# Optimization experiments

Measured on AMD Instinct MI355X. Metric: run time of the kernel, lower is better.

Reference implementation:

```python
import jax, jax.numpy as jnp
import numpy as np


def setup_inputs() -> dict:
    key = jax.random.key(0)
    k1, k2, k3, k4, k5 = jax.random.split(key, 5)
    B, N, E, C, O = 4, 10000, 32, 128, 128
    x = jax.random.normal(k1, (B, N, C), dtype=jnp.float32)
    idx = jax.random.randint(k2, (B, N, E), 0, N)
    drop = jax.random.uniform(k3, (B, N, E)) < 0.1
    edge_index = jnp.where(drop, -1, idx).astype(jnp.int64)
    W = jax.random.normal(k4, (2 * C, O), dtype=jnp.float32) * (1.0 / np.sqrt(2 * C))
    b = jax.random.normal(k5, (O,), dtype=jnp.float32) * 0.01
    return {"x": x, "edge_index": edge_index, "W": W, "b": b}


def reference(x, edge_index, W, b):
    B, N, C = x.shape
    E = edge_index.shape[-1]
    # pad a zero node row; -1 indices point at it (torch negative-index semantics)
    padded = jnp.concatenate([x, jnp.zeros((B, 1, C), dtype=x.dtype)], axis=1)  # [B, N+1, C]
    idx = jnp.where(edge_index < 0, N, edge_index)
    neigh = jax.vmap(lambda p, i: p[i])(padded, idx)  # [B, N, E, C]
    x_e = jnp.broadcast_to(x[:, :, None, :], (B, N, E, C))
    feat = jnp.concatenate([x_e, neigh - x_e], axis=-1)  # [B, N, E, 2C]
    h = jax.nn.elu(jnp.einsum('bnec,co->bneo', feat, W) + b)  # [B, N, E, O]
    h = jnp.where((edge_index != -1)[..., None], h, -jnp.inf)
    return jnp.max(h, axis=2)  # [B, N, O]
```

## Files before the change

### kernel.cpp

```cpp
#include <hip/hip_runtime.h>
#include <math.h>

#define BATCH 4
#define NNODE 10000
#define EDIM  32
#define CDIM  128
#define ODIM  128
#define MTOT  (BATCH * NNODE)

typedef __attribute__((ext_vector_type(8))) short bf16x8;
typedef __attribute__((ext_vector_type(4))) float f32x4;

#define SENT_BF16 0xFBFFu

__device__ __forceinline__ unsigned short f2bf(float f) {
    unsigned u = __float_as_uint(f);
    u += 0x7fffu + ((u >> 16) & 1u);
    return (unsigned short)(u >> 16);
}
__device__ __forceinline__ float bf2f(unsigned short h) {
    return __uint_as_float(((unsigned)h) << 16);
}
__device__ __forceinline__ void pkmax(unsigned& acc, unsigned v) {
    asm("v_pk_max_f16 %0, %0, %1" : "+v"(acc) : "v"(v));
}

__global__ __launch_bounds__(256) void prep_w(
    const float* __restrict__ W, unsigned short* __restrict__ Bcat,
    unsigned short* __restrict__ Tsent)
{
    int gid = blockIdx.x * 256 + threadIdx.x;
    int n = gid >> 7;
    int k = gid & 127;
    float v;
    if (n < 128) v = W[(size_t)k * ODIM + n] - W[(size_t)(k + 128) * ODIM + n];
    else         v = W[(size_t)(k + 128) * ODIM + (n - 128)];
    Bcat[(size_t)n * CDIM + k] = f2bf(v);
    if (gid < ODIM) Tsent[gid] = (unsigned short)SENT_BF16;
}

__global__ __launch_bounds__(256) void gemm_mfma(
    const float* __restrict__ x,
    const unsigned short* __restrict__ Bcat,
    const float* __restrict__ bias,
    unsigned short* __restrict__ U,
    unsigned short* __restrict__ T)
{
    __shared__ unsigned short As[32 * 128];

    const int tid  = threadIdx.x;
    const int m0   = blockIdx.x * 32;
    const int wv   = tid >> 6;
    const int lane = tid & 63;
    const int l16  = lane & 15;
    const int quad = lane >> 4;
    const int nq   = wv * 64;

    #pragma unroll
    for (int i = 0; i < 4; i++) {
        int lin = i * 256 + tid;
        int row = lin >> 5;
        int f4  = lin & 31;
        float4 v = *(const float4*)&x[(size_t)(m0 + row) * CDIM + f4 * 4];
        ushort4 h;
        h.x = f2bf(v.x); h.y = f2bf(v.y); h.z = f2bf(v.z); h.w = f2bf(v.w);
        int kblk = f4 >> 1, half = f4 & 1;
        *(ushort4*)((char*)As + row * 256 + (((kblk ^ (row & 15)) << 4) + half * 8)) = h;
    }
    __syncthreads();

    f32x4 acc[2][4];
    #pragma unroll
    for (int i = 0; i < 2; i++)
        #pragma unroll
        for (int j = 0; j < 4; j++) acc[i][j] = (f32x4){0.f, 0.f, 0.f, 0.f};

    #pragma unroll
    for (int ks = 0; ks < 4; ks++) {
        const int kb = ks * 32 + quad * 8;

        bf16x8 wfr[4];
        #pragma unroll
        for (int ct = 0; ct < 4; ct++)
            wfr[ct] = *(const bf16x8*)(Bcat + (size_t)(nq + ct * 16 + l16) * CDIM + kb);

        bf16x8 xfr[2];
        #pragma unroll
        for (int rt = 0; rt < 2; rt++) {
            int row  = rt * 16 + l16;
            int kblk = ks * 4 + quad;
            xfr[rt] = *(const bf16x8*)((char*)As + row * 256 + ((kblk ^ l16) << 4));
        }

        #pragma unroll
        for (int rt = 0; rt < 2; rt++)
            #pragma unroll
            for (int ct = 0; ct < 4; ct++)
                acc[rt][ct] = __builtin_amdgcn_mfma_f32_16x16x32_bf16(
                    wfr[ct], xfr[rt], acc[rt][ct], 0, 0, 0);
    }

    if (wv < 2) {
        #pragma unroll
        for (int ct = 0; ct < 4; ct++) {
            int c0 = nq + ct * 16 + quad * 4;
            float4 b4 = *(const float4*)&bias[c0];
            #pragma unroll
            for (int rt = 0; rt < 2; rt++) {
                int row = m0 + rt * 16 + l16;
                ushort4 h;
                h.x = f2bf(acc[rt][ct][0] + b4.x);
                h.y = f2bf(acc[rt][ct][1] + b4.y);
                h.z = f2bf(acc[rt][ct][2] + b4.z);
                h.w = f2bf(acc[rt][ct][3] + b4.w);
                *(ushort4*)&U[(size_t)row * ODIM + c0] = h;
            }
        }
    } else {
        #pragma unroll
        for (int ct = 0; ct < 4; ct++) {
            int c0 = (nq - 128) + ct * 16 + quad * 4;
            #pragma unroll
            for (int rt = 0; rt < 2; rt++) {
                int row = m0 + rt * 16 + l16;
                ushort4 h;
                h.x = f2bf(acc[rt][ct][0]);
                h.y = f2bf(acc[rt][ct][1]);
                h.z = f2bf(acc[rt][ct][2]);
                h.w = f2bf(acc[rt][ct][3]);
                *(ushort4*)&T[(size_t)row * ODIM + c0] = h;
            }
        }
    }
}

__global__ __launch_bounds__(256) void gather_max(
    const int* __restrict__ idx,
    const unsigned short* __restrict__ Ub,
    const unsigned short* __restrict__ T,
    float* __restrict__ out)
{
    __shared__ int sidx[16][EDIM];

    const int g   = blockIdx.x;
    const int b   = g & 3;
    const int nb0 = (g >> 2) * 16;
    const int tid = threadIdx.x;
    const int sent = NNODE * (BATCH - b);

    #pragma unroll
    for (int i = 0; i < 2; i++) {
        int lin = i * 256 + tid;
        int n = lin >> 5, e = lin & 31;
        int j = idx[(size_t)(b * NNODE + nb0 + n) * EDIM + e];
        sidx[n][e] = (j < 0) ? sent : j;
    }
    __syncthreads();

    const int wv   = tid >> 6;
    const int lane = tid & 63;
    const int q4   = lane >> 4;
    const int l16  = lane & 15;
    const int myn  = wv * 4 + q4;
    const int node = b * NNODE + nb0 + myn;
    const unsigned short* tb = T + (size_t)b * NNODE * ODIM;
    const int o8 = l16 * 8;

    uint4 uraw = *(const uint4*)(Ub + (size_t)node * ODIM + o8);

    const unsigned SENT2 = (SENT_BF16 << 16) | SENT_BF16;
    unsigned m01 = SENT2, m23 = SENT2, m45 = SENT2, m67 = SENT2;

    #pragma unroll
    for (int e0 = 0; e0 < EDIM; e0 += 16) {
        uint4 v[16];
        #pragma unroll
        for (int q = 0; q < 16; q++) {
            int j = sidx[myn][e0 + q];
            v[q] = *(const uint4*)(tb + (size_t)j * ODIM + o8);
        }
        #pragma unroll
        for (int q = 0; q < 16; q++) {
            pkmax(m01, v[q].x);
            pkmax(m23, v[q].y);
            pkmax(m45, v[q].z);
            pkmax(m67, v[q].w);
        }
    }

    const bool any = (m01 & 0xffffu) != SENT_BF16;
    float m[8];
    m[0] = bf2f((unsigned short)(m01 & 0xffff)); m[1] = bf2f((unsigned short)(m01 >> 16));
    m[2] = bf2f((unsigned short)(m23 & 0xffff)); m[3] = bf2f((unsigned short)(m23 >> 16));
    m[4] = bf2f((unsigned short)(m45 & 0xffff)); m[5] = bf2f((unsigned short)(m45 >> 16));
    m[6] = bf2f((unsigned short)(m67 & 0xffff)); m[7] = bf2f((unsigned short)(m67 >> 16));
    float uu[8];
    uu[0] = bf2f((unsigned short)(uraw.x & 0xffff)); uu[1] = bf2f((unsigned short)(uraw.x >> 16));
    uu[2] = bf2f((unsigned short)(uraw.y & 0xffff)); uu[3] = bf2f((unsigned short)(uraw.y >> 16));
    uu[4] = bf2f((unsigned short)(uraw.z & 0xffff)); uu[5] = bf2f((unsigned short)(uraw.z >> 16));
    uu[6] = bf2f((unsigned short)(uraw.w & 0xffff)); uu[7] = bf2f((unsigned short)(uraw.w >> 16));
    float r[8];
    #pragma unroll
    for (int i = 0; i < 8; i++) {
        float s = uu[i] + m[i];
        r[i] = any ? (s > 0.f ? s : __expf(s) - 1.f) : -INFINITY;
    }
    *(float4*)&out[(size_t)node * ODIM + o8]     = make_float4(r[0], r[1], r[2], r[3]);
    *(float4*)&out[(size_t)node * ODIM + o8 + 4] = make_float4(r[4], r[5], r[6], r[7]);
}

extern "C" void kernel_launch(void* const* d_in, const int* in_sizes, int n_in,
                              void* d_out, int out_size, void* d_ws, size_t ws_size,
                              hipStream_t stream) {
    const float* x    = (const float*)d_in[0];
    const int*   idx  = (const int*)d_in[1];
    const float* W    = (const float*)d_in[2];
    const float* bias = (const float*)d_in[3];
    float* out        = (float*)d_out;

    const size_t tBytes = (size_t)(MTOT + 1) * ODIM * sizeof(unsigned short);
    const size_t uBytes = (size_t)MTOT * ODIM * sizeof(unsigned short);
    unsigned short* T    = (unsigned short*)d_ws;
    unsigned short* U    = (unsigned short*)((char*)d_ws + tBytes);
    unsigned short* Bcat = (unsigned short*)((char*)d_ws + tBytes + uBytes);
    unsigned short* Tsent = T + (size_t)MTOT * ODIM;

    prep_w    <<<128,        256, 0, stream>>>(W, Bcat, Tsent);
    gemm_mfma <<<MTOT / 32,  256, 0, stream>>>(x, Bcat, bias, U, T);
    gather_max<<<MTOT / 16,  256, 0, stream>>>(idx, U, T, out);
}
```

Before: 112.5 us.

## Fuse GEMM and gather into persistent cooperative kernel with grid sync

Merges the GEMM and gather-max kernels into one persistent cooperative kernel. Blocks loop over GEMM tiles, meet at a grid-wide barrier, then loop over gather tiles, which removes one kernel launch and the boundary between the two. It also adds an occupancy query on the host for every call. The grid is capped at 1024 blocks, and if the cooperative launch fails the code falls back to two separate launches.

```diff
diff --git a/kernel.cpp b/kernel.cpp
--- a/kernel.cpp
+++ b/kernel.cpp
@@ -1,5 +1,8 @@
 #include <hip/hip_runtime.h>
+#include <hip/hip_cooperative_groups.h>
 #include <math.h>
+
+namespace cg = cooperative_groups;
 
 #define BATCH 4
 #define NNODE 10000
@@ -7,6 +10,8 @@
 #define CDIM  128
 #define ODIM  128
 #define MTOT  (BATCH * NNODE)
+#define NT_GEMM   1250
+#define NT_GATHER 2500
 
 typedef __attribute__((ext_vector_type(8))) short bf16x8;
 typedef __attribute__((ext_vector_type(4))) float f32x4;
@@ -39,17 +44,13 @@
     if (gid < ODIM) Tsent[gid] = (unsigned short)SENT_BF16;
 }
 
-__global__ __launch_bounds__(256) void gemm_mfma(
-    const float* __restrict__ x,
-    const unsigned short* __restrict__ Bcat,
+__device__ __forceinline__ void gemm_tile(
+    int t, int tid, unsigned short* As,
+    const float* __restrict__ x, const unsigned short* __restrict__ Bcat,
     const float* __restrict__ bias,
-    unsigned short* __restrict__ U,
-    unsigned short* __restrict__ T)
-{
-    __shared__ unsigned short As[32 * 128];
-
-    const int tid  = threadIdx.x;
-    const int m0   = blockIdx.x * 32;
+    unsigned short* __restrict__ U, unsigned short* __restrict__ T)
+{
+    const int m0   = t * 32;
     const int wv   = tid >> 6;
     const int lane = tid & 63;
     const int l16  = lane & 15;
@@ -78,12 +79,10 @@
     #pragma unroll
     for (int ks = 0; ks < 4; ks++) {
         const int kb = ks * 32 + quad * 8;
-
         bf16x8 wfr[4];
         #pragma unroll
         for (int ct = 0; ct < 4; ct++)
             wfr[ct] = *(const bf16x8*)(Bcat + (size_t)(nq + ct * 16 + l16) * CDIM + kb);
-
         bf16x8 xfr[2];
         #pragma unroll
         for (int rt = 0; rt < 2; rt++) {
@@ -91,7 +90,6 @@
             int kblk = ks * 4 + quad;
             xfr[rt] = *(const bf16x8*)((char*)As + row * 256 + ((kblk ^ l16) << 4));
         }
-
         #pragma unroll
         for (int rt = 0; rt < 2; rt++)
             #pragma unroll
@@ -134,18 +132,13 @@
     }
 }
 
-__global__ __launch_bounds__(256) void gather_max(
-    const int* __restrict__ idx,
-    const unsigned short* __restrict__ Ub,
-    const unsigned short* __restrict__ T,
-    float* __restrict__ out)
-{
-    __shared__ int sidx[16][EDIM];
-
-    const int g   = blockIdx.x;
+__device__ __forceinline__ void gather_tile(
+    int g, int tid, int (*sidx)[EDIM],
+    const int* __restrict__ idx, const unsigned short* __restrict__ Ub,
+    const unsigned short* __restrict__ T, float* __restrict__ out)
+{
     const int b   = g & 3;
     const int nb0 = (g >> 2) * 16;
-    const int tid = threadIdx.x;
     const int sent = NNODE * (BATCH - b);
 
     #pragma unroll
@@ -181,10 +174,8 @@
         }
         #pragma unroll
         for (int q = 0; q < 16; q++) {
-            pkmax(m01, v[q].x);
-            pkmax(m23, v[q].y);
-            pkmax(m45, v[q].z);
-            pkmax(m67, v[q].w);
+            pkmax(m01, v[q].x); pkmax(m23, v[q].y);
+            pkmax(m45, v[q].z); pkmax(m67, v[q].w);
         }
     }
 
@@ -209,6 +200,45 @@
     *(float4*)&out[(size_t)node * ODIM + o8 + 4] = make_float4(r[4], r[5], r[6], r[7]);
 }
 
+__global__ __launch_bounds__(256, 4) void fused(
+    const float* __restrict__ x, const unsigned short* __restrict__ Bcat,
+    const float* __restrict__ bias, unsigned short* __restrict__ U,
+    unsigned short* __restrict__ T, const int* __restrict__ idx,
+    float* __restrict__ out)
+{
+    __shared__ __align__(16) unsigned short smem[32 * 128];
+    const int tid = threadIdx.x;
+
+    for (int t = blockIdx.x; t < NT_GEMM; t += gridDim.x) {
+        __syncthreads();
+        gemm_tile(t, tid, smem, x, Bcat, bias, U, T);
+    }
+
+    cg::this_grid().sync();
+
+    int (*sidx)[EDIM] = (int(*)[EDIM])smem;
+    for (int t = blockIdx.x; t < NT_GATHER; t += gridDim.x) {
+        __syncthreads();
+        gather_tile(t, tid, sidx, idx, U, T, out);
+    }
+}
+
+__global__ __launch_bounds__(256) void gemm_fb(
+    const float* __restrict__ x, const unsigned short* __restrict__ Bcat,
+    const float* __restrict__ bias, unsigned short* __restrict__ U,
+    unsigned short* __restrict__ T)
+{
+    __shared__ __align__(16) unsigned short smem[32 * 128];
+    gemm_tile(blockIdx.x, threadIdx.x, smem, x, Bcat, bias, U, T);
+}
+__global__ __launch_bounds__(256) void gather_fb(
+    const int* __restrict__ idx, const unsigned short* __restrict__ Ub,
+    const unsigned short* __restrict__ T, float* __restrict__ out)
+{
+    __shared__ int sidx[16][EDIM];
+    gather_tile(blockIdx.x, threadIdx.x, sidx, idx, Ub, T, out);
+}
+
 extern "C" void kernel_launch(void* const* d_in, const int* in_sizes, int n_in,
                               void* d_out, int out_size, void* d_ws, size_t ws_size,
                               hipStream_t stream) {
@@ -225,7 +255,23 @@
     unsigned short* Bcat = (unsigned short*)((char*)d_ws + tBytes + uBytes);
     unsigned short* Tsent = T + (size_t)MTOT * ODIM;
 
-    prep_w    <<<128,        256, 0, stream>>>(W, Bcat, Tsent);
-    gemm_mfma <<<MTOT / 32,  256, 0, stream>>>(x, Bcat, bias, U, T);
-    gather_max<<<MTOT / 16,  256, 0, stream>>>(idx, U, T, out);
-}
+    prep_w<<<128, 256, 0, stream>>>(W, Bcat, Tsent);
+
+    int perCU = 0;
+    hipError_t qerr = hipOccupancyMaxActiveBlocksPerMultiprocessor(
+        &perCU, (const void*)fused, 256, 0);
+    int grid = (qerr == hipSuccess && perCU >= 1) ? perCU * 256 : 0;
+    if (grid > 1024) grid = 1024;
+
+    hipError_t lerr = hipErrorUnknown;
+    if (grid >= 8) {
+        void* args[7] = {(void*)&x, (void*)&Bcat, (void*)&bias, (void*)&U,
+                         (void*)&T, (void*)&idx, (void*)&out};
+        lerr = hipLaunchCooperativeKernel((const void*)fused, dim3(grid),
+                                          dim3(256), args, 0, stream);
+    }
+    if (lerr != hipSuccess) {
+        gemm_fb  <<<NT_GEMM,   256, 0, stream>>>(x, Bcat, bias, U, T);
+        gather_fb<<<NT_GATHER, 256, 0, stream>>>(idx, U, T, out);
+    }
+}
```

After: 199.8 us. 77.5% more time.

## Fuse U-projection GEMM into gather-max kernel and shrink T-only GEMM

Applied to the files above, without the earlier changes.

The first GEMM now computes only the T half (neighbor projection) with 64-row tiles. The U half (center projection plus bias) is recomputed inside the gather kernel via MFMA on the block's 16 nodes and kept in fp32 shared memory. This removes the U write/read round trip through global memory and its bf16 rounding, at the cost of re-reading x in the gather kernel and extra LDS and sync there. Neighbor indices are now biased to global row numbers, with a single global sentinel row.

```diff
diff --git a/kernel.cpp b/kernel.cpp
--- a/kernel.cpp
+++ b/kernel.cpp
@@ -7,6 +7,7 @@
 #define CDIM  128
 #define ODIM  128
 #define MTOT  (BATCH * NNODE)
+#define SENTROW MTOT
 
 typedef __attribute__((ext_vector_type(8))) short bf16x8;
 typedef __attribute__((ext_vector_type(4))) float f32x4;
@@ -39,25 +40,23 @@
     if (gid < ODIM) Tsent[gid] = (unsigned short)SENT_BF16;
 }
 
-__global__ __launch_bounds__(256) void gemm_mfma(
+__global__ __launch_bounds__(256) void gemm_t(
     const float* __restrict__ x,
     const unsigned short* __restrict__ Bcat,
-    const float* __restrict__ bias,
-    unsigned short* __restrict__ U,
     unsigned short* __restrict__ T)
 {
-    __shared__ unsigned short As[32 * 128];
+    __shared__ unsigned short As[64 * 128];
 
     const int tid  = threadIdx.x;
-    const int m0   = blockIdx.x * 32;
+    const int m0   = blockIdx.x * 64;
     const int wv   = tid >> 6;
     const int lane = tid & 63;
     const int l16  = lane & 15;
     const int quad = lane >> 4;
-    const int nq   = wv * 64;
-
-    #pragma unroll
-    for (int i = 0; i < 4; i++) {
+    const int nq   = wv * 32;
+
+    #pragma unroll
+    for (int i = 0; i < 8; i++) {
         int lin = i * 256 + tid;
         int row = lin >> 5;
         int f4  = lin & 31;
@@ -69,104 +68,119 @@
     }
     __syncthreads();
 
-    f32x4 acc[2][4];
-    #pragma unroll
-    for (int i = 0; i < 2; i++)
-        #pragma unroll
-        for (int j = 0; j < 4; j++) acc[i][j] = (f32x4){0.f, 0.f, 0.f, 0.f};
+    f32x4 acc[4][2];
+    #pragma unroll
+    for (int i = 0; i < 4; i++)
+        #pragma unroll
+        for (int j = 0; j < 2; j++) acc[i][j] = (f32x4){0.f, 0.f, 0.f, 0.f};
 
     #pragma unroll
     for (int ks = 0; ks < 4; ks++) {
         const int kb = ks * 32 + quad * 8;
-
-        bf16x8 wfr[4];
-        #pragma unroll
-        for (int ct = 0; ct < 4; ct++)
-            wfr[ct] = *(const bf16x8*)(Bcat + (size_t)(nq + ct * 16 + l16) * CDIM + kb);
-
-        bf16x8 xfr[2];
-        #pragma unroll
-        for (int rt = 0; rt < 2; rt++) {
+        bf16x8 wfr[2];
+        #pragma unroll
+        for (int ct = 0; ct < 2; ct++)
+            wfr[ct] = *(const bf16x8*)(Bcat + (size_t)(128 + nq + ct * 16 + l16) * CDIM + kb);
+        bf16x8 xfr[4];
+        #pragma unroll
+        for (int rt = 0; rt < 4; rt++) {
             int row  = rt * 16 + l16;
             int kblk = ks * 4 + quad;
             xfr[rt] = *(const bf16x8*)((char*)As + row * 256 + ((kblk ^ l16) << 4));
         }
-
-        #pragma unroll
-        for (int rt = 0; rt < 2; rt++)
+        #pragma unroll
+        for (int rt = 0; rt < 4; rt++)
             #pragma unroll
-            for (int ct = 0; ct < 4; ct++)
+            for (int ct = 0; ct < 2; ct++)
                 acc[rt][ct] = __builtin_amdgcn_mfma_f32_16x16x32_bf16(
                     wfr[ct], xfr[rt], acc[rt][ct], 0, 0, 0);
     }
 
-    if (wv < 2) {
-        #pragma unroll
-        for (int ct = 0; ct < 4; ct++) {
-            int c0 = nq + ct * 16 + quad * 4;
-            float4 b4 = *(const float4*)&bias[c0];
-            #pragma unroll
-            for (int rt = 0; rt < 2; rt++) {
-                int row = m0 + rt * 16 + l16;
-                ushort4 h;
-                h.x = f2bf(acc[rt][ct][0] + b4.x);
-                h.y = f2bf(acc[rt][ct][1] + b4.y);
-                h.z = f2bf(acc[rt][ct][2] + b4.z);
-                h.w = f2bf(acc[rt][ct][3] + b4.w);
-                *(ushort4*)&U[(size_t)row * ODIM + c0] = h;
-            }
-        }
-    } else {
-        #pragma unroll
-        for (int ct = 0; ct < 4; ct++) {
-            int c0 = (nq - 128) + ct * 16 + quad * 4;
-            #pragma unroll
-            for (int rt = 0; rt < 2; rt++) {
-                int row = m0 + rt * 16 + l16;
-                ushort4 h;
-                h.x = f2bf(acc[rt][ct][0]);
-                h.y = f2bf(acc[rt][ct][1]);
-                h.z = f2bf(acc[rt][ct][2]);
-                h.w = f2bf(acc[rt][ct][3]);
-                *(ushort4*)&T[(size_t)row * ODIM + c0] = h;
-            }
-        }
-    }
-}
-
-__global__ __launch_bounds__(256) void gather_max(
+    #pragma unroll
+    for (int ct = 0; ct < 2; ct++) {
+        int c0 = nq + ct * 16 + quad * 4;
+        #pragma unroll
+        for (int rt = 0; rt < 4; rt++) {
+            int row = m0 + rt * 16 + l16;
+            ushort4 h;
+            h.x = f2bf(acc[rt][ct][0]);
+            h.y = f2bf(acc[rt][ct][1]);
+            h.z = f2bf(acc[rt][ct][2]);
+            h.w = f2bf(acc[rt][ct][3]);
+            *(ushort4*)&T[(size_t)row * ODIM + c0] = h;
+        }
+    }
+}
+
+__global__ __launch_bounds__(256) void fused_ug(
+    const float* __restrict__ x,
+    const unsigned short* __restrict__ Bcat,
+    const float* __restrict__ bias,
     const int* __restrict__ idx,
-    const unsigned short* __restrict__ Ub,
     const unsigned short* __restrict__ T,
     float* __restrict__ out)
 {
-    __shared__ int sidx[16][EDIM];
-
-    const int g   = blockIdx.x;
-    const int b   = g & 3;
-    const int nb0 = (g >> 2) * 16;
-    const int tid = threadIdx.x;
-    const int sent = NNODE * (BATCH - b);
+    __shared__ unsigned short As[16 * 128];
+    __shared__ float Uf[16 * 132];
+    __shared__ int sidx[16][EDIM + 1];
+
+    const int bid  = blockIdx.x;
+    const int b    = bid & 3;
+    const int nb0  = (bid >> 2) * 16;
+    const int m0   = b * NNODE + nb0;
+    const int tid  = threadIdx.x;
+    const int wv   = tid >> 6;
+    const int lane = tid & 63;
+    const int l16  = lane & 15;
+    const int quad = lane >> 4;
+    const int nq   = wv * 32;
 
     #pragma unroll
     for (int i = 0; i < 2; i++) {
         int lin = i * 256 + tid;
-        int n = lin >> 5, e = lin & 31;
-        int j = idx[(size_t)(b * NNODE + nb0 + n) * EDIM + e];
-        sidx[n][e] = (j < 0) ? sent : j;
+        int row = lin >> 5;
+        int f4  = lin & 31;
+        float4 v = *(const float4*)&x[(size_t)(m0 + row) * CDIM + f4 * 4];
+        ushort4 h;
+        h.x = f2bf(v.x); h.y = f2bf(v.y); h.z = f2bf(v.z); h.w = f2bf(v.w);
+        int kblk = f4 >> 1, half = f4 & 1;
+        *(ushort4*)((char*)As + row * 256 + (((kblk ^ row) << 4) + half * 8)) = h;
+        int j = idx[(size_t)(m0 + row) * EDIM + f4];
+        sidx[row][f4] = (j < 0) ? SENTROW : b * NNODE + j;
     }
     __syncthreads();
 
-    const int wv   = tid >> 6;
-    const int lane = tid & 63;
-    const int q4   = lane >> 4;
-    const int l16  = lane & 15;
-    const int myn  = wv * 4 + q4;
-    const int node = b * NNODE + nb0 + myn;
-    const unsigned short* tb = T + (size_t)b * NNODE * ODIM;
-    const int o8 = l16 * 8;
-
-    uint4 uraw = *(const uint4*)(Ub + (size_t)node * ODIM + o8);
+    f32x4 acc[2];
+    acc[0] = (f32x4){0.f, 0.f, 0.f, 0.f};
+    acc[1] = (f32x4){0.f, 0.f, 0.f, 0.f};
+    #pragma unroll
+    for (int ks = 0; ks < 4; ks++) {
+        const int kb = ks * 32 + quad * 8;
+        bf16x8 wfr[2];
+        #pragma unroll
+        for (int ct = 0; ct < 2; ct++)
+            wfr[ct] = *(const bf16x8*)(Bcat + (size_t)(nq + ct * 16 + l16) * CDIM + kb);
+        int kblk = ks * 4 + quad;
+        bf16x8 xfr = *(const bf16x8*)((char*)As + l16 * 256 + ((kblk ^ l16) << 4));
+        #pragma unroll
+        for (int ct = 0; ct < 2; ct++)
+            acc[ct] = __builtin_amdgcn_mfma_f32_16x16x32_bf16(
+                wfr[ct], xfr, acc[ct], 0, 0, 0);
+    }
+    #pragma unroll
+    for (int ct = 0; ct < 2; ct++) {
+        int c0 = nq + ct * 16 + quad * 4;
+        float4 b4 = *(const float4*)&bias[c0];
+        *(float4*)&Uf[l16 * 132 + c0] = make_float4(
+            acc[ct][0] + b4.x, acc[ct][1] + b4.y,
+            acc[ct][2] + b4.z, acc[ct][3] + b4.w);
+    }
+    __syncthreads();
+
+    const int myn  = tid >> 4;
+    const int hl   = tid & 15;
+    const int node = m0 + myn;
+    const int o8   = hl * 8;
 
     const unsigned SENT2 = (SENT_BF16 << 16) | SENT_BF16;
     unsigned m01 = SENT2, m23 = SENT2, m45 = SENT2, m67 = SENT2;
@@ -177,14 +191,12 @@
         #pragma unroll
         for (int q = 0; q < 16; q++) {
             int j = sidx[myn][e0 + q];
-            v[q] = *(const uint4*)(tb + (size_t)j * ODIM + o8);
+            v[q] = *(const uint4*)(T + (size_t)j * ODIM + o8);
         }
         #pragma unroll
         for (int q = 0; q < 16; q++) {
-            pkmax(m01, v[q].x);
-            pkmax(m23, v[q].y);
-            pkmax(m45, v[q].z);
-            pkmax(m67, v[q].w);
+            pkmax(m01, v[q].x); pkmax(m23, v[q].y);
+            pkmax(m45, v[q].z); pkmax(m67, v[q].w);
         }
     }
 
@@ -194,11 +206,10 @@
     m[2] = bf2f((unsigned short)(m23 & 0xffff)); m[3] = bf2f((unsigned short)(m23 >> 16));
     m[4] = bf2f((unsigned short)(m45 & 0xffff)); m[5] = bf2f((unsigned short)(m45 >> 16));
     m[6] = bf2f((unsigned short)(m67 & 0xffff)); m[7] = bf2f((unsigned short)(m67 >> 16));
-    float uu[8];
-    uu[0] = bf2f((unsigned short)(uraw.x & 0xffff)); uu[1] = bf2f((unsigned short)(uraw.x >> 16));
-    uu[2] = bf2f((unsigned short)(uraw.y & 0xffff)); uu[3] = bf2f((unsigned short)(uraw.y >> 16));
-    uu[4] = bf2f((unsigned short)(uraw.z & 0xffff)); uu[5] = bf2f((unsigned short)(uraw.z >> 16));
-    uu[6] = bf2f((unsigned short)(uraw.w & 0xffff)); uu[7] = bf2f((unsigned short)(uraw.w >> 16));
+
+    float4 u0 = *(const float4*)&Uf[myn * 132 + o8];
+    float4 u1 = *(const float4*)&Uf[myn * 132 + o8 + 4];
+    float uu[8] = {u0.x, u0.y, u0.z, u0.w, u1.x, u1.y, u1.z, u1.w};
     float r[8];
     #pragma unroll
     for (int i = 0; i < 8; i++) {
@@ -219,13 +230,11 @@
     float* out        = (float*)d_out;
 
     const size_t tBytes = (size_t)(MTOT + 1) * ODIM * sizeof(unsigned short);
-    const size_t uBytes = (size_t)MTOT * ODIM * sizeof(unsigned short);
-    unsigned short* T    = (unsigned short*)d_ws;
-    unsigned short* U    = (unsigned short*)((char*)d_ws + tBytes);
-    unsigned short* Bcat = (unsigned short*)((char*)d_ws + tBytes + uBytes);
+    unsigned short* T     = (unsigned short*)d_ws;
+    unsigned short* Bcat  = (unsigned short*)((char*)d_ws + tBytes);
     unsigned short* Tsent = T + (size_t)MTOT * ODIM;
 
-    prep_w    <<<128,        256, 0, stream>>>(W, Bcat, Tsent);
-    gemm_mfma <<<MTOT / 32,  256, 0, stream>>>(x, Bcat, bias, U, T);
-    gather_max<<<MTOT / 16,  256, 0, stream>>>(idx, U, T, out);
-}
+    prep_w  <<<128,       256, 0, stream>>>(W, Bcat, Tsent);
+    gemm_t  <<<MTOT / 64, 256, 0, stream>>>(x, Bcat, T);
+    fused_ug<<<MTOT / 16, 256, 0, stream>>>(x, Bcat, bias, idx, T, out);
+}
```

Result: no change. 111.3 us (-1.1%).
